# Performance work log

Measured on AMD Instinct MI355X. Metric: run time of the kernel, lower is better.

The kernel has to match this reference:

```python
import jax, jax.numpy as jnp
import numpy as np
import math

D = 128       # d_model (file-scope constant)
L_LEN = 128   # length; forced == d_model by the un-transposed attention call
NH = 4        # n_head
DK = D // NH
K = 7         # depthwise conv kernel size
LC = 4        # conv_num
EPS = 1e-5    # LayerNorm eps
NEG = -1e30


def _pos_encoding():
    i = np.arange(D).astype(np.float64)
    freqs = np.where(i % 2 == 0, 10000.0 ** (-i / D), -(10000.0 ** ((1 - i) / D)))
    phases = np.where(i % 2 == 0, 0.0, math.pi / 2)
    pos = np.arange(L_LEN).astype(np.float64)[None, :]          # (1, L)
    pe = np.sin(pos * freqs[:, None] + phases[:, None])          # (D, L)
    return jnp.asarray(pe, jnp.float32)

PE = _pos_encoding()


def layernorm2d(x, w, b):
    # LayerNorm over the trailing (D, L) dims jointly, elementwise affine (D, L)
    mu = x.mean(axis=(-2, -1), keepdims=True)
    var = x.var(axis=(-2, -1), keepdims=True)
    return (x - mu) * jax.lax.rsqrt(var + EPS) * w + b


def sep_conv(x, dw_w, dw_b, pw_w, pw_b):
    # depthwise conv1d (groups=C) then 1x1 pointwise conv. x: (B, C, L)
    h = jax.lax.conv_general_dilated(
        x, dw_w[:, None, :], window_strides=(1,), padding=[(K // 2, K // 2)],
        dimension_numbers=('NCH', 'OIH', 'NCH'), feature_group_count=D)
    h = h + dw_b[:, None]
    return jnp.einsum('bcl,oc->bol', h, pw_w) + pw_b[:, None]


def mha(x, mask_f, Wq, bq, Wk, bk, Wv, bv, Wo, bo):
    # x: (B, Lx, F) with Lx == F == D here (module feeds (B, d_model, length) untransposed)
    B, Lx, _ = x.shape
    q = (x @ Wq.T + bq).reshape(B, Lx, NH, DK)
    k = (x @ Wk.T + bk).reshape(B, Lx, NH, DK)
    v = (x @ Wv.T + bv).reshape(B, Lx, NH, DK)
    scores = jnp.einsum('bqhd,bkhd->bhqk', q, k) * (1.0 / math.sqrt(DK))
    m = mask_f[:, None, None, :]                         # (B,1,1,Lx)
    scores = scores * (1.0 - m) + m * NEG                # mask_logits
    attn = jax.nn.softmax(scores, axis=-1)
    out = jnp.einsum('bhqk,bkhd->bqhd', attn, v).reshape(B, Lx, D)
    return out @ Wo.T + bo


def setup_inputs() -> dict:
    key = jax.random.key(0)
    ks = jax.random.split(key, 16)
    B = 1024
    s = 0.02
    inp = {
        'x': jax.random.normal(ks[0], (B, D, L_LEN), jnp.float32),
        'mask': jax.random.randint(ks[1], (B, L_LEN), 0, 2, jnp.int32),
        'dw_w': jax.random.normal(ks[2], (LC, D, K), jnp.float32) * s,
        'dw_b': jnp.zeros((LC, D), jnp.float32),
        'pw_w': jax.random.normal(ks[3], (LC, D, D), jnp.float32) * s,
        'pw_b': jnp.zeros((LC, D), jnp.float32),
        'normb_w': jnp.ones((D, L_LEN), jnp.float32),
        'normb_b': jnp.zeros((D, L_LEN), jnp.float32),
        'norms_w': jnp.ones((LC, D, L_LEN), jnp.float32),
        'norms_b': jnp.zeros((LC, D, L_LEN), jnp.float32),
        'norme_w': jnp.ones((D, L_LEN), jnp.float32),
        'norme_b': jnp.zeros((D, L_LEN), jnp.float32),
        'Wq': jax.random.normal(ks[4], (D, D), jnp.float32) * s,
        'bq': jnp.zeros((D,), jnp.float32),
        'Wk': jax.random.normal(ks[5], (D, D), jnp.float32) * s,
        'bk': jnp.zeros((D,), jnp.float32),
        'Wv': jax.random.normal(ks[6], (D, D), jnp.float32) * s,
        'bv': jnp.zeros((D,), jnp.float32),
        'Wo': jax.random.normal(ks[7], (D, D), jnp.float32) * s,
        'bo': jnp.zeros((D,), jnp.float32),
        'fc_w': jax.random.normal(ks[8], (D, D), jnp.float32) * s,
        'fc_b': jnp.zeros((D,), jnp.float32),
    }
    return inp


def reference(x, mask, dw_w, dw_b, pw_w, pw_b, normb_w, normb_b, norms_w, norms_b,
              norme_w, norme_b, Wq, bq, Wk, bk, Wv, bv, Wo, bo, fc_w, fc_b):
    # Eval mode: all dropouts are identity.
    mask_f = mask.astype(x.dtype)
    out = x + PE                                  # PosEncoder
    res = out
    out = layernorm2d(out, normb_w, normb_b)      # normb
    for i in range(LC):                           # fixed small layer loop
        h = sep_conv(out, dw_w[i], dw_b[i], pw_w[i], pw_b[i])
        out = jax.nn.relu(h) + res
        res = out
        out = layernorm2d(out, norms_w[i], norms_b[i])
    att = mha(out, mask_f, Wq, bq, Wk, bk, Wv, bv, Wo, bo)
    out = att + res
    res = out
    out = layernorm2d(out, norme_w, norme_b)
    # fc applied over channel dim: (B,C,L)->(B,L,C) linear ->(B,C,L)
    h = jnp.einsum('bcl,oc->bol', out, fc_w) + fc_b[:, None]
    out = jax.nn.relu(h) + res
    return out
```

## Files before the change

### kernel.cpp

```cpp
#include <hip/hip_runtime.h>

#define NEGF -1e30f
#define EPSF 1e-5f

typedef __attribute__((ext_vector_type(8))) short bf16x8;
typedef __attribute__((ext_vector_type(4))) float f32x4;
typedef unsigned short u16;
typedef unsigned int u32;

#define WSU_PW 0
#define WSU_FC 65536
#define WSU_WO 81920
#define WSU_WQ 98304
#define WSU_WK 114688
#define WSU_WV 131072
#define WSU_END 147456

__device__ __forceinline__ u16 f2bf(float x) {
  u32 u = __float_as_uint(x);
  u += 0x7fffu + ((u >> 16) & 1u);
  return (u16)(u >> 16);
}
__device__ __forceinline__ float bf2f(u16 u) {
  return __uint_as_float(((u32)u) << 16);
}
__device__ __forceinline__ f32x4 mfma16(bf16x8 a, bf16x8 b, f32x4 c) {
  return __builtin_amdgcn_mfma_f32_16x16x32_bf16(a, b, c, 0, 0, 0);
}
__device__ __forceinline__ void mm_frags(const u16* base, bf16x8* f) {
  f[0] = *(const bf16x8*)(base);
  f[1] = *(const bf16x8*)(base + 32);
  f[2] = *(const bf16x8*)(base + 64);
  f[3] = *(const bf16x8*)(base + 96);
}

__global__ __launch_bounds__(128) void prep_kernel(
    const float* __restrict__ pw_w, const float* __restrict__ fc_w,
    const float* __restrict__ Wo, const float* __restrict__ Wq,
    const float* __restrict__ Wk, const float* __restrict__ Wv,
    u16* __restrict__ wsu) {
  int job = blockIdx.x, r = blockIdx.y, c = threadIdx.x;
  int idx = r * 128 + c;
  if (job < 4)       wsu[WSU_PW + job * 16384 + idx] = f2bf(pw_w[job * 16384 + idx]);
  else if (job == 4) wsu[WSU_FC + idx] = f2bf(fc_w[idx]);
  else if (job == 5) wsu[WSU_WO + idx] = f2bf(Wo[idx]);
  else if (job == 6) wsu[WSU_WQ + idx] = f2bf(Wq[idx]);
  else if (job == 7) wsu[WSU_WK + idx] = f2bf(Wk[idx]);
  else if (job == 8) wsu[WSU_WV + idx] = f2bf(Wv[idx]);
  else {
    float* pe = (float*)(wsu + WSU_END);
    int d = r, pos = c;
    double freq, phase;
    if ((d & 1) == 0) { freq = pow(10000.0, -(double)d / 128.0); phase = 0.0; }
    else { freq = -pow(10000.0, (1.0 - (double)d) / 128.0); phase = 1.5707963267948966; }
    pe[d * 128 + pos] = (float)sin((double)pos * freq + phase);
  }
}

__device__ __forceinline__ void ln_stats(const float* resv, float* red, int t,
                                         float& mu, float& inv) {
  float s = 0.f, s2 = 0.f;
#pragma unroll
  for (int i = 0; i < 16; i++) { float v = resv[i]; s += v; s2 += v * v; }
#pragma unroll
  for (int off = 32; off > 0; off >>= 1) {
    s += __shfl_down(s, off, 64);
    s2 += __shfl_down(s2, off, 64);
  }
  if ((t & 63) == 0) { red[(t >> 6) * 2] = s; red[(t >> 6) * 2 + 1] = s2; }
  __syncthreads();
  float S = 0.f, S2 = 0.f;
#pragma unroll
  for (int i = 0; i < 16; i++) { S += red[2 * i]; S2 += red[2 * i + 1]; }
  mu = S * (1.0f / 16384.0f);
  float var = S2 * (1.0f / 16384.0f) - mu * mu;
  inv = rsqrtf(var + EPSF);
}

__global__ __launch_bounds__(1024) void enc_kernel(
    const float* __restrict__ x, const int* __restrict__ mask,
    const float* __restrict__ dw_w, const float* __restrict__ dw_b,
    const float* __restrict__ pw_b,
    const float* __restrict__ normb_w, const float* __restrict__ normb_b,
    const float* __restrict__ norms_w, const float* __restrict__ norms_b,
    const float* __restrict__ norme_w, const float* __restrict__ norme_b,
    const float* __restrict__ bq, const float* __restrict__ bk,
    const float* __restrict__ bv, const float* __restrict__ bo,
    const float* __restrict__ fc_b, const u16* __restrict__ wsu,
    const float* __restrict__ pe, float* __restrict__ out) {
  __shared__ __align__(16) u16 A_raw[128 * 136 + 16];
  __shared__ __align__(16) u16 VTb[32 * 136];
  __shared__ float EX[512];
  __shared__ float mask_s[128];
  __shared__ float red[32];
  u16* A = A_raw + 8;
  u16* QH = A;
  u16* KH = A + 5120;
  u16* PN = A;

  const int t = threadIdx.x;
  const int b = blockIdx.x;
  const int lane = t & 63;
  const int r16 = lane & 15;
  const int quad = lane >> 4;
  const int wv = t >> 6;
  const int m0 = __builtin_amdgcn_readfirstlane((wv >> 1) << 4);
  const int nh = __builtin_amdgcn_readfirstlane(wv & 1);
  const int l = t & 127;
  const int og = __builtin_amdgcn_readfirstlane(t >> 7);
  const int obase = og << 4;
  const int dup = __builtin_amdgcn_readfirstlane(wv >> 3);
  const int mq0 = __builtin_amdgcn_readfirstlane((wv & 7) << 4);

  if (t < 128) mask_s[t] = (float)mask[b * 128 + t];

  float res[16];
  {
    const float* xb = x + (size_t)b * 16384;
#pragma unroll
    for (int i = 0; i < 16; i++) {
      int o = obase + i;
      res[i] = xb[o * 128 + l] + pe[o * 128 + l];
    }
  }
  {
    float mu, inv;
    ln_stats(res, red, t, mu, inv);
#pragma unroll
    for (int i = 0; i < 16; i++) {
      int o = obase + i;
      A[o * 136 + l] = f2bf((res[i] - mu) * inv * normb_w[o * 128 + l] + normb_b[o * 128 + l]);
    }
    __syncthreads();
  }

#pragma unroll 1
  for (int layer = 0; layer < 4; layer++) {
    {
      const float* dwp = dw_w + layer * 896 + l * 7;
      float wreg[7];
#pragma unroll
      for (int j = 0; j < 7; j++) wreg[j] = dwp[j];
      float bias = dw_b[layer * 128 + l];
      const u16* xrow = A + l * 136;
      const int lb = og << 4;
      bf16x8 vz = {0, 0, 0, 0, 0, 0, 0, 0};
      bf16x8 v0 = (lb == 0) ? vz : *(const bf16x8*)(xrow + lb - 8);
      bf16x8 v1 = *(const bf16x8*)(xrow + lb);
      bf16x8 v2 = *(const bf16x8*)(xrow + lb + 8);
      bf16x8 v3 = (lb == 112) ? vz : *(const bf16x8*)(xrow + lb + 16);
      __syncthreads();
#pragma unroll
      for (int k = 0; k < 2; k++) {
        bf16x8 vp = k ? v1 : v0;
        bf16x8 vc = k ? v2 : v1;
        bf16x8 vn = k ? v3 : v2;
        float w14[14];
        w14[0] = bf2f((u16)vp[5]); w14[1] = bf2f((u16)vp[6]); w14[2] = bf2f((u16)vp[7]);
#pragma unroll
        for (int j = 0; j < 8; j++) w14[3 + j] = bf2f((u16)vc[j]);
        w14[11] = bf2f((u16)vn[0]); w14[12] = bf2f((u16)vn[1]); w14[13] = bf2f((u16)vn[2]);
        const int lb2 = lb + 8 * k;
#pragma unroll
        for (int j = 0; j < 8; j++) {
          float a = bias;
#pragma unroll
          for (int tt = 0; tt < 7; tt++) a += w14[j + tt] * wreg[tt];
          A[(lb2 + j) * 136 + l] = f2bf(a);
        }
      }
    }
    __syncthreads();
    {
      const u16* pwp = wsu + WSU_PW + (layer << 14) + (m0 + r16) * 128 + quad * 8;
      bf16x8 a[4];
      mm_frags(pwp, a);
      f32x4 c4[4];
#pragma unroll
      for (int ni = 0; ni < 4; ni++) {
        int n = nh * 4 + ni;
        const u16* hb = A + (16 * n + r16) * 136 + quad * 8;
        f32x4 c = {0.f, 0.f, 0.f, 0.f};
        c = mfma16(a[0], *(const bf16x8*)(hb), c);
        c = mfma16(a[1], *(const bf16x8*)(hb + 32), c);
        c = mfma16(a[2], *(const bf16x8*)(hb + 64), c);
        c = mfma16(a[3], *(const bf16x8*)(hb + 96), c);
        c4[ni] = c;
      }
      __syncthreads();
#pragma unroll
      for (int ni = 0; ni < 4; ni++) {
        int n = nh * 4 + ni;
        u16* sp = A + (m0 + quad * 4) * 136 + 16 * n + r16;
        sp[0] = f2bf(c4[ni][0]); sp[136] = f2bf(c4[ni][1]);
        sp[272] = f2bf(c4[ni][2]); sp[408] = f2bf(c4[ni][3]);
      }
    }
    __syncthreads();
    {
#pragma unroll
      for (int i = 0; i < 16; i++)
        res[i] += fmaxf(bf2f(A[(obase + i) * 136 + l]) + pw_b[layer * 128 + obase + i], 0.f);
      float mu, inv;
      ln_stats(res, red, t, mu, inv);
      const float* wg = norms_w + layer * 16384;
      const float* bg = norms_b + layer * 16384;
#pragma unroll
      for (int i = 0; i < 16; i++) {
        int o = obase + i;
        A[o * 136 + l] = f2bf((res[i] - mu) * inv * wg[o * 128 + l] + bg[o * 128 + l]);
      }
      __syncthreads();
    }
  }

  bf16x8 xf[4];
  mm_frags(A + (m0 + r16) * 136 + quad * 8, xf);
  __syncthreads();

  u32 att32[8];
#pragma unroll 1
  for (int hd = 0; hd < 4; hd++) {
    {
      const int j2 = nh * 16 + r16;
      const int jrow = hd * 32 + j2;
      {
        bf16x8 w[4];
        mm_frags(wsu + WSU_WQ + jrow * 128 + quad * 8, w);
        f32x4 c = {0.f, 0.f, 0.f, 0.f};
        c = mfma16(xf[0], w[0], c); c = mfma16(xf[1], w[1], c);
        c = mfma16(xf[2], w[2], c); c = mfma16(xf[3], w[3], c);
        float bb = bq[jrow];
#pragma unroll
        for (int r = 0; r < 4; r++)
          QH[(m0 + quad * 4 + r) * 40 + j2] = f2bf((c[r] + bb) * 0.17677669529663687f);
      }
      {
        bf16x8 w[4];
        mm_frags(wsu + WSU_WK + jrow * 128 + quad * 8, w);
        f32x4 c = {0.f, 0.f, 0.f, 0.f};
        c = mfma16(xf[0], w[0], c); c = mfma16(xf[1], w[1], c);
        c = mfma16(xf[2], w[2], c); c = mfma16(xf[3], w[3], c);
        float bb = bk[jrow];
#pragma unroll
        for (int r = 0; r < 4; r++)
          KH[(m0 + quad * 4 + r) * 40 + j2] = f2bf(c[r] + bb);
      }
      {
        bf16x8 w[4];
        mm_frags(wsu + WSU_WV + jrow * 128 + quad * 8, w);
        f32x4 c = {0.f, 0.f, 0.f, 0.f};
        c = mfma16(xf[0], w[0], c); c = mfma16(xf[1], w[1], c);
        c = mfma16(xf[2], w[2], c); c = mfma16(xf[3], w[3], c);
        float bb = bv[jrow];
        u32 lo = (u32)f2bf(c[0] + bb) | ((u32)f2bf(c[1] + bb) << 16);
        u32 hi = (u32)f2bf(c[2] + bb) | ((u32)f2bf(c[3] + bb) << 16);
        u16* vp = VTb + j2 * 136 + m0 + quad * 4;
        *(u32*)(vp) = lo;
        *(u32*)(vp + 2) = hi;
      }
    }
    __syncthreads();
    f32x4 sc[4];
    {
      bf16x8 aq = *(const bf16x8*)(QH + (mq0 + r16) * 40 + quad * 8);
#pragma unroll
      for (int ni = 0; ni < 4; ni++) {
        f32x4 z = {0.f, 0.f, 0.f, 0.f};
        sc[ni] = mfma16(aq, *(const bf16x8*)(KH + ((dup * 4 + ni) * 16 + r16) * 40 + quad * 8), z);
      }
#pragma unroll
      for (int ni = 0; ni < 4; ni++) {
        float mv = mask_s[(dup * 4 + ni) * 16 + r16];
        if (mv > 0.5f) { sc[ni][0] = NEGF; sc[ni][1] = NEGF; sc[ni][2] = NEGF; sc[ni][3] = NEGF; }
      }
    }
    float mxr[4];
#pragma unroll
    for (int r = 0; r < 4; r++) {
      float mx = fmaxf(fmaxf(sc[0][r], sc[1][r]), fmaxf(sc[2][r], sc[3][r]));
      mx = fmaxf(mx, __shfl_xor(mx, 1, 64));
      mx = fmaxf(mx, __shfl_xor(mx, 2, 64));
      mx = fmaxf(mx, __shfl_xor(mx, 4, 64));
      mx = fmaxf(mx, __shfl_xor(mx, 8, 64));
      if (r16 == 0) EX[dup * 128 + mq0 + quad * 4 + r] = mx;
      mxr[r] = mx;
    }
    __syncthreads();
    float ps[4];
#pragma unroll
    for (int r = 0; r < 4; r++) {
      const int row = mq0 + quad * 4 + r;
      float fm = fmaxf(mxr[r], EX[(dup ^ 1) * 128 + row]);
      float s = 0.f;
      u16* pp2 = PN + row * 136 + r16;
#pragma unroll
      for (int ni = 0; ni < 4; ni++) {
        float p = __expf(sc[ni][r] - fm);
        pp2[(dup * 4 + ni) * 16] = f2bf(p);
        s += p;
      }
      s += __shfl_xor(s, 1, 64);
      s += __shfl_xor(s, 2, 64);
      s += __shfl_xor(s, 4, 64);
      s += __shfl_xor(s, 8, 64);
      if (r16 == 0) EX[256 + dup * 128 + row] = s;
      ps[r] = s;
    }
    __syncthreads();
    {
      const u16* pq = PN + (mq0 + r16) * 136 + quad * 8;
      const u16* vb = VTb + (dup * 16 + r16) * 136 + quad * 8;
      f32x4 c = {0.f, 0.f, 0.f, 0.f};
      c = mfma16(*(const bf16x8*)(pq), *(const bf16x8*)(vb), c);
      c = mfma16(*(const bf16x8*)(pq + 32), *(const bf16x8*)(vb + 32), c);
      c = mfma16(*(const bf16x8*)(pq + 64), *(const bf16x8*)(vb + 64), c);
      c = mfma16(*(const bf16x8*)(pq + 96), *(const bf16x8*)(vb + 96), c);
      float v0 = c[0] / (ps[0] + EX[256 + (dup ^ 1) * 128 + mq0 + quad * 4 + 0]);
      float v1 = c[1] / (ps[1] + EX[256 + (dup ^ 1) * 128 + mq0 + quad * 4 + 1]);
      float v2 = c[2] / (ps[2] + EX[256 + (dup ^ 1) * 128 + mq0 + quad * 4 + 2]);
      float v3 = c[3] / (ps[3] + EX[256 + (dup ^ 1) * 128 + mq0 + quad * 4 + 3]);
      att32[hd * 2 + 0] = (u32)f2bf(v0) | ((u32)f2bf(v1) << 16);
      att32[hd * 2 + 1] = (u32)f2bf(v2) | ((u32)f2bf(v3) << 16);
    }
    __syncthreads();
  }

#pragma unroll
  for (int hd = 0; hd < 4; hd++)
#pragma unroll
    for (int i = 0; i < 2; i++)
#pragma unroll
      for (int h = 0; h < 2; h++)
        A[(mq0 + quad * 4 + 2 * i + h) * 136 + hd * 32 + dup * 16 + r16] =
            (u16)(att32[hd * 2 + i] >> (16 * h));
  __syncthreads();
  {
    const u16* ap = A + (m0 + r16) * 136 + quad * 8;
    bf16x8 a4[4];
    mm_frags(ap, a4);
    f32x4 c4[4];
#pragma unroll
    for (int ni = 0; ni < 4; ni++) {
      int n = nh * 4 + ni;
      bf16x8 w[4];
      mm_frags(wsu + WSU_WO + (16 * n + r16) * 128 + quad * 8, w);
      f32x4 c = {0.f, 0.f, 0.f, 0.f};
      c = mfma16(a4[0], w[0], c); c = mfma16(a4[1], w[1], c);
      c = mfma16(a4[2], w[2], c); c = mfma16(a4[3], w[3], c);
      c4[ni] = c;
    }
    __syncthreads();
#pragma unroll
    for (int ni = 0; ni < 4; ni++) {
      int n = nh * 4 + ni;
      u16* sp = A + (m0 + quad * 4) * 136 + 16 * n + r16;
      sp[0] = f2bf(c4[ni][0]); sp[136] = f2bf(c4[ni][1]);
      sp[272] = f2bf(c4[ni][2]); sp[408] = f2bf(c4[ni][3]);
    }
  }
  __syncthreads();
  {
    float bol = bo[l];
#pragma unroll
    for (int i = 0; i < 16; i++) res[i] += bf2f(A[(obase + i) * 136 + l]) + bol;
    float mu, inv;
    ln_stats(res, red, t, mu, inv);
#pragma unroll
    for (int i = 0; i < 16; i += 2) {
      int o = obase + i;
      float v0 = (res[i] - mu) * inv * norme_w[o * 128 + l] + norme_b[o * 128 + l];
      float v1 = (res[i + 1] - mu) * inv * norme_w[(o + 1) * 128 + l] + norme_b[(o + 1) * 128 + l];
      *(u32*)(A + l * 136 + o) = (u32)f2bf(v0) | ((u32)f2bf(v1) << 16);
    }
    __syncthreads();
  }
  {
    const u16* fp = wsu + WSU_FC + (m0 + r16) * 128 + quad * 8;
    bf16x8 a4[4];
    mm_frags(fp, a4);
    f32x4 c4[4];
#pragma unroll
    for (int ni = 0; ni < 4; ni++) {
      int n = nh * 4 + ni;
      const u16* hb = A + (16 * n + r16) * 136 + quad * 8;
      f32x4 c = {0.f, 0.f, 0.f, 0.f};
      c = mfma16(a4[0], *(const bf16x8*)(hb), c);
      c = mfma16(a4[1], *(const bf16x8*)(hb + 32), c);
      c = mfma16(a4[2], *(const bf16x8*)(hb + 64), c);
      c = mfma16(a4[3], *(const bf16x8*)(hb + 96), c);
      c4[ni] = c;
    }
    __syncthreads();
#pragma unroll
    for (int ni = 0; ni < 4; ni++) {
      int n = nh * 4 + ni;
      u16* sp = A + (m0 + quad * 4) * 136 + 16 * n + r16;
      sp[0] = f2bf(c4[ni][0]); sp[136] = f2bf(c4[ni][1]);
      sp[272] = f2bf(c4[ni][2]); sp[408] = f2bf(c4[ni][3]);
    }
  }
  __syncthreads();
  {
    float* outb = out + (size_t)b * 16384;
#pragma unroll
    for (int i = 0; i < 16; i++) {
      float hv = bf2f(A[(obase + i) * 136 + l]) + fc_b[obase + i];
      outb[(obase + i) * 128 + l] = fmaxf(hv, 0.f) + res[i];
    }
  }
}

extern "C" void kernel_launch(void* const* d_in, const int* in_sizes, int n_in,
                              void* d_out, int out_size, void* d_ws, size_t ws_size,
                              hipStream_t stream) {
  const float* x       = (const float*)d_in[0];
  const int*   mask    = (const int*)d_in[1];
  const float* dw_w    = (const float*)d_in[2];
  const float* dw_b    = (const float*)d_in[3];
  const float* pw_w    = (const float*)d_in[4];
  const float* pw_b    = (const float*)d_in[5];
  const float* normb_w = (const float*)d_in[6];
  const float* normb_b = (const float*)d_in[7];
  const float* norms_w = (const float*)d_in[8];
  const float* norms_b = (const float*)d_in[9];
  const float* norme_w = (const float*)d_in[10];
  const float* norme_b = (const float*)d_in[11];
  const float* Wq      = (const float*)d_in[12];
  const float* bq      = (const float*)d_in[13];
  const float* Wk      = (const float*)d_in[14];
  const float* bk      = (const float*)d_in[15];
  const float* Wv      = (const float*)d_in[16];
  const float* bv      = (const float*)d_in[17];
  const float* Wo      = (const float*)d_in[18];
  const float* bo      = (const float*)d_in[19];
  const float* fc_w    = (const float*)d_in[20];
  const float* fc_b    = (const float*)d_in[21];
  float* out = (float*)d_out;
  u16* wsu = (u16*)d_ws;
  const float* pe = (const float*)(wsu + WSU_END);
  int B = in_sizes[0] / 16384;

  prep_kernel<<<dim3(10, 128), dim3(128), 0, stream>>>(pw_w, fc_w, Wo, Wq, Wk, Wv, wsu);
  enc_kernel<<<dim3(B), dim3(1024), 0, stream>>>(
      x, mask, dw_w, dw_b, pw_b, normb_w, normb_b, norms_w, norms_b,
      norme_w, norme_b, bq, bk, bv, bo, fc_b, wsu, pe, out);
}
```

Measured before the change: 644.4 us.

## Process two batch elements per block to amortize barriers and weight fragments

Each 1024-thread block now handles two batch samples at once, with duplicated LDS buffers (activations, conv scratch, V^T, softmax stats, masks). Every stage is interleaved across both samples: LayerNorm reductions share one barrier, the depthwise conv writes to separate scratch buffers so a barrier is dropped, and GEMM weight fragments (pointwise, QKV, Wo, fc) are loaded once and reused for both samples. The aim is to halve barrier and weight-load overhead per sample and give each wave more independent MFMA work. In exchange LDS use roughly doubles and register pressure rises, which may reduce occupancy or cause spills, and the grid is halved to 512 blocks.

```diff
diff --git a/kernel.cpp b/kernel.cpp
--- a/kernel.cpp
+++ b/kernel.cpp
@@ -57,24 +57,248 @@
   }
 }
 
-__device__ __forceinline__ void ln_stats(const float* resv, float* red, int t,
-                                         float& mu, float& inv) {
-  float s = 0.f, s2 = 0.f;
-#pragma unroll
-  for (int i = 0; i < 16; i++) { float v = resv[i]; s += v; s2 += v * v; }
+__device__ __forceinline__ void ln_stats2(const float* r0, const float* r1,
+                                          float* red0, float* red1, int t,
+                                          float& mu0, float& inv0,
+                                          float& mu1, float& inv1) {
+  float s0 = 0.f, q0 = 0.f, s1 = 0.f, q1 = 0.f;
+#pragma unroll
+  for (int i = 0; i < 16; i++) {
+    float a = r0[i], b = r1[i];
+    s0 += a; q0 += a * a; s1 += b; q1 += b * b;
+  }
 #pragma unroll
   for (int off = 32; off > 0; off >>= 1) {
-    s += __shfl_down(s, off, 64);
-    s2 += __shfl_down(s2, off, 64);
-  }
-  if ((t & 63) == 0) { red[(t >> 6) * 2] = s; red[(t >> 6) * 2 + 1] = s2; }
+    s0 += __shfl_down(s0, off, 64); q0 += __shfl_down(q0, off, 64);
+    s1 += __shfl_down(s1, off, 64); q1 += __shfl_down(q1, off, 64);
+  }
+  if ((t & 63) == 0) {
+    int w = t >> 6;
+    red0[w * 2] = s0; red0[w * 2 + 1] = q0;
+    red1[w * 2] = s1; red1[w * 2 + 1] = q1;
+  }
   __syncthreads();
-  float S = 0.f, S2 = 0.f;
-#pragma unroll
-  for (int i = 0; i < 16; i++) { S += red[2 * i]; S2 += red[2 * i + 1]; }
-  mu = S * (1.0f / 16384.0f);
-  float var = S2 * (1.0f / 16384.0f) - mu * mu;
-  inv = rsqrtf(var + EPSF);
+  float S0 = 0.f, Q0 = 0.f, S1 = 0.f, Q1 = 0.f;
+#pragma unroll
+  for (int i = 0; i < 16; i++) {
+    S0 += red0[2 * i]; Q0 += red0[2 * i + 1];
+    S1 += red1[2 * i]; Q1 += red1[2 * i + 1];
+  }
+  mu0 = S0 * (1.0f / 16384.0f);
+  float v0 = Q0 * (1.0f / 16384.0f) - mu0 * mu0; inv0 = rsqrtf(v0 + EPSF);
+  mu1 = S1 * (1.0f / 16384.0f);
+  float v1 = Q1 * (1.0f / 16384.0f) - mu1 * mu1; inv1 = rsqrtf(v1 + EPSF);
+}
+
+__device__ __forceinline__ void dw_conv(const u16* A, u16* XS, const float* wreg,
+                                        float bias, int og, int l) {
+  const u16* xrow = A + l * 136;
+  const int lb = og << 4;
+  bf16x8 vz = {0, 0, 0, 0, 0, 0, 0, 0};
+  bf16x8 v0 = (lb == 0) ? vz : *(const bf16x8*)(xrow + lb - 8);
+  bf16x8 v1 = *(const bf16x8*)(xrow + lb);
+  bf16x8 v2 = *(const bf16x8*)(xrow + lb + 8);
+  bf16x8 v3 = (lb == 112) ? vz : *(const bf16x8*)(xrow + lb + 16);
+#pragma unroll
+  for (int k = 0; k < 2; k++) {
+    bf16x8 vp = k ? v1 : v0;
+    bf16x8 vc = k ? v2 : v1;
+    bf16x8 vn = k ? v3 : v2;
+    float w14[14];
+    w14[0] = bf2f((u16)vp[5]); w14[1] = bf2f((u16)vp[6]); w14[2] = bf2f((u16)vp[7]);
+#pragma unroll
+    for (int j = 0; j < 8; j++) w14[3 + j] = bf2f((u16)vc[j]);
+    w14[11] = bf2f((u16)vn[0]); w14[12] = bf2f((u16)vn[1]); w14[13] = bf2f((u16)vn[2]);
+    const int lb2 = lb + 8 * k;
+#pragma unroll
+    for (int j = 0; j < 8; j++) {
+      float a = bias;
+#pragma unroll
+      for (int tt = 0; tt < 7; tt++) a += w14[j + tt] * wreg[tt];
+      XS[(lb2 + j) * 136 + l] = f2bf(a);
+    }
+  }
+}
+
+__device__ __forceinline__ void gemm_stage2(const u16* aB, int aS,
+                                            const u16* b0B, const u16* b1B, int bS,
+                                            u16* d0, u16* d1,
+                                            int m0, int nh, int r16, int quad) {
+  bf16x8 a[4];
+  mm_frags(aB + (m0 + r16) * aS + quad * 8, a);
+#pragma unroll
+  for (int ni = 0; ni < 4; ni++) {
+    int n = nh * 4 + ni;
+    {
+      bf16x8 w[4];
+      mm_frags(b0B + (16 * n + r16) * bS + quad * 8, w);
+      f32x4 c = {0.f, 0.f, 0.f, 0.f};
+      c = mfma16(a[0], w[0], c); c = mfma16(a[1], w[1], c);
+      c = mfma16(a[2], w[2], c); c = mfma16(a[3], w[3], c);
+      u16* sp = d0 + (m0 + quad * 4) * 136 + 16 * n + r16;
+      sp[0] = f2bf(c[0]); sp[136] = f2bf(c[1]); sp[272] = f2bf(c[2]); sp[408] = f2bf(c[3]);
+    }
+    {
+      bf16x8 w[4];
+      mm_frags(b1B + (16 * n + r16) * bS + quad * 8, w);
+      f32x4 c = {0.f, 0.f, 0.f, 0.f};
+      c = mfma16(a[0], w[0], c); c = mfma16(a[1], w[1], c);
+      c = mfma16(a[2], w[2], c); c = mfma16(a[3], w[3], c);
+      u16* sp = d1 + (m0 + quad * 4) * 136 + 16 * n + r16;
+      sp[0] = f2bf(c[0]); sp[136] = f2bf(c[1]); sp[272] = f2bf(c[2]); sp[408] = f2bf(c[3]);
+    }
+  }
+}
+
+__device__ __forceinline__ void gemm_stage2b(const u16* a0B, const u16* a1B, int aS,
+                                             const u16* bB, int bS,
+                                             u16* d0, u16* d1,
+                                             int m0, int nh, int r16, int quad) {
+  bf16x8 a0[4], a1[4];
+  mm_frags(a0B + (m0 + r16) * aS + quad * 8, a0);
+  mm_frags(a1B + (m0 + r16) * aS + quad * 8, a1);
+#pragma unroll
+  for (int ni = 0; ni < 4; ni++) {
+    int n = nh * 4 + ni;
+    bf16x8 w[4];
+    mm_frags(bB + (16 * n + r16) * bS + quad * 8, w);
+    {
+      f32x4 c = {0.f, 0.f, 0.f, 0.f};
+      c = mfma16(a0[0], w[0], c); c = mfma16(a0[1], w[1], c);
+      c = mfma16(a0[2], w[2], c); c = mfma16(a0[3], w[3], c);
+      u16* sp = d0 + (m0 + quad * 4) * 136 + 16 * n + r16;
+      sp[0] = f2bf(c[0]); sp[136] = f2bf(c[1]); sp[272] = f2bf(c[2]); sp[408] = f2bf(c[3]);
+    }
+    {
+      f32x4 c = {0.f, 0.f, 0.f, 0.f};
+      c = mfma16(a1[0], w[0], c); c = mfma16(a1[1], w[1], c);
+      c = mfma16(a1[2], w[2], c); c = mfma16(a1[3], w[3], c);
+      u16* sp = d1 + (m0 + quad * 4) * 136 + 16 * n + r16;
+      sp[0] = f2bf(c[0]); sp[136] = f2bf(c[1]); sp[272] = f2bf(c[2]); sp[408] = f2bf(c[3]);
+    }
+  }
+}
+
+__device__ __forceinline__ void qkv2(const u16* XS0, const u16* XS1,
+                                     u16* QH0, u16* QH1, u16* KH0, u16* KH1,
+                                     u16* VT0, u16* VT1,
+                                     const u16* wsu, int jrow,
+                                     float bqv, float bkv, float bvv,
+                                     int m0, int j2, int r16, int quad) {
+  bf16x8 x0[4], x1[4];
+  mm_frags(XS0 + (m0 + r16) * 136 + quad * 8, x0);
+  mm_frags(XS1 + (m0 + r16) * 136 + quad * 8, x1);
+  {
+    bf16x8 w[4];
+    mm_frags(wsu + WSU_WQ + jrow * 128 + quad * 8, w);
+    f32x4 c0 = {0.f, 0.f, 0.f, 0.f}, c1 = {0.f, 0.f, 0.f, 0.f};
+    c0 = mfma16(x0[0], w[0], c0); c0 = mfma16(x0[1], w[1], c0);
+    c0 = mfma16(x0[2], w[2], c0); c0 = mfma16(x0[3], w[3], c0);
+    c1 = mfma16(x1[0], w[0], c1); c1 = mfma16(x1[1], w[1], c1);
+    c1 = mfma16(x1[2], w[2], c1); c1 = mfma16(x1[3], w[3], c1);
+#pragma unroll
+    for (int r = 0; r < 4; r++) {
+      QH0[(m0 + quad * 4 + r) * 40 + j2] = f2bf((c0[r] + bqv) * 0.17677669529663687f);
+      QH1[(m0 + quad * 4 + r) * 40 + j2] = f2bf((c1[r] + bqv) * 0.17677669529663687f);
+    }
+  }
+  {
+    bf16x8 w[4];
+    mm_frags(wsu + WSU_WK + jrow * 128 + quad * 8, w);
+    f32x4 c0 = {0.f, 0.f, 0.f, 0.f}, c1 = {0.f, 0.f, 0.f, 0.f};
+    c0 = mfma16(x0[0], w[0], c0); c0 = mfma16(x0[1], w[1], c0);
+    c0 = mfma16(x0[2], w[2], c0); c0 = mfma16(x0[3], w[3], c0);
+    c1 = mfma16(x1[0], w[0], c1); c1 = mfma16(x1[1], w[1], c1);
+    c1 = mfma16(x1[2], w[2], c1); c1 = mfma16(x1[3], w[3], c1);
+#pragma unroll
+    for (int r = 0; r < 4; r++) {
+      KH0[(m0 + quad * 4 + r) * 40 + j2] = f2bf(c0[r] + bkv);
+      KH1[(m0 + quad * 4 + r) * 40 + j2] = f2bf(c1[r] + bkv);
+    }
+  }
+  {
+    bf16x8 w[4];
+    mm_frags(wsu + WSU_WV + jrow * 128 + quad * 8, w);
+    f32x4 c0 = {0.f, 0.f, 0.f, 0.f}, c1 = {0.f, 0.f, 0.f, 0.f};
+    c0 = mfma16(x0[0], w[0], c0); c0 = mfma16(x0[1], w[1], c0);
+    c0 = mfma16(x0[2], w[2], c0); c0 = mfma16(x0[3], w[3], c0);
+    c1 = mfma16(x1[0], w[0], c1); c1 = mfma16(x1[1], w[1], c1);
+    c1 = mfma16(x1[2], w[2], c1); c1 = mfma16(x1[3], w[3], c1);
+    u16* vp0 = VT0 + j2 * 136 + m0 + quad * 4;
+    u16* vp1 = VT1 + j2 * 136 + m0 + quad * 4;
+    *(u32*)(vp0) = (u32)f2bf(c0[0] + bvv) | ((u32)f2bf(c0[1] + bvv) << 16);
+    *(u32*)(vp0 + 2) = (u32)f2bf(c0[2] + bvv) | ((u32)f2bf(c0[3] + bvv) << 16);
+    *(u32*)(vp1) = (u32)f2bf(c1[0] + bvv) | ((u32)f2bf(c1[1] + bvv) << 16);
+    *(u32*)(vp1 + 2) = (u32)f2bf(c1[2] + bvv) | ((u32)f2bf(c1[3] + bvv) << 16);
+  }
+}
+
+__device__ __forceinline__ void mha_scores(const u16* QH, const u16* KH, const float* msk,
+                                           float* EX, int dup, int mq0, int r16, int quad,
+                                           f32x4 (&sc)[4], float (&mxr)[4]) {
+  bf16x8 aq = *(const bf16x8*)(QH + (mq0 + r16) * 40 + quad * 8);
+#pragma unroll
+  for (int ni = 0; ni < 4; ni++) {
+    f32x4 z = {0.f, 0.f, 0.f, 0.f};
+    sc[ni] = mfma16(aq, *(const bf16x8*)(KH + ((dup * 4 + ni) * 16 + r16) * 40 + quad * 8), z);
+  }
+#pragma unroll
+  for (int ni = 0; ni < 4; ni++) {
+    float mv = msk[(dup * 4 + ni) * 16 + r16];
+    if (mv > 0.5f) { sc[ni][0] = NEGF; sc[ni][1] = NEGF; sc[ni][2] = NEGF; sc[ni][3] = NEGF; }
+  }
+#pragma unroll
+  for (int r = 0; r < 4; r++) {
+    float mx = fmaxf(fmaxf(sc[0][r], sc[1][r]), fmaxf(sc[2][r], sc[3][r]));
+    mx = fmaxf(mx, __shfl_xor(mx, 1, 64));
+    mx = fmaxf(mx, __shfl_xor(mx, 2, 64));
+    mx = fmaxf(mx, __shfl_xor(mx, 4, 64));
+    mx = fmaxf(mx, __shfl_xor(mx, 8, 64));
+    if (r16 == 0) EX[dup * 128 + mq0 + quad * 4 + r] = mx;
+    mxr[r] = mx;
+  }
+}
+
+__device__ __forceinline__ void mha_exp(u16* PN, float* EX, const f32x4 (&sc)[4],
+                                        const float (&mxr)[4], int dup, int mq0,
+                                        int r16, int quad, float (&ps)[4]) {
+#pragma unroll
+  for (int r = 0; r < 4; r++) {
+    const int row = mq0 + quad * 4 + r;
+    float fm = fmaxf(mxr[r], EX[(dup ^ 1) * 128 + row]);
+    float s = 0.f;
+    u16* pp = PN + row * 136 + r16;
+#pragma unroll
+    for (int ni = 0; ni < 4; ni++) {
+      float p = __expf(sc[ni][r] - fm);
+      pp[(dup * 4 + ni) * 16] = f2bf(p);
+      s += p;
+    }
+    s += __shfl_xor(s, 1, 64);
+    s += __shfl_xor(s, 2, 64);
+    s += __shfl_xor(s, 4, 64);
+    s += __shfl_xor(s, 8, 64);
+    if (r16 == 0) EX[256 + dup * 128 + row] = s;
+    ps[r] = s;
+  }
+}
+
+__device__ __forceinline__ void mha_pv(const u16* PN, const u16* VT, const float* EX,
+                                       const float (&ps)[4], int dup, int mq0,
+                                       int r16, int quad, u32& alo, u32& ahi) {
+  const u16* pq = PN + (mq0 + r16) * 136 + quad * 8;
+  const u16* vb = VT + (dup * 16 + r16) * 136 + quad * 8;
+  f32x4 c = {0.f, 0.f, 0.f, 0.f};
+  c = mfma16(*(const bf16x8*)(pq), *(const bf16x8*)(vb), c);
+  c = mfma16(*(const bf16x8*)(pq + 32), *(const bf16x8*)(vb + 32), c);
+  c = mfma16(*(const bf16x8*)(pq + 64), *(const bf16x8*)(vb + 64), c);
+  c = mfma16(*(const bf16x8*)(pq + 96), *(const bf16x8*)(vb + 96), c);
+  float v0 = c[0] / (ps[0] + EX[256 + (dup ^ 1) * 128 + mq0 + quad * 4 + 0]);
+  float v1 = c[1] / (ps[1] + EX[256 + (dup ^ 1) * 128 + mq0 + quad * 4 + 1]);
+  float v2 = c[2] / (ps[2] + EX[256 + (dup ^ 1) * 128 + mq0 + quad * 4 + 2]);
+  float v3 = c[3] / (ps[3] + EX[256 + (dup ^ 1) * 128 + mq0 + quad * 4 + 3]);
+  alo = (u32)f2bf(v0) | ((u32)f2bf(v1) << 16);
+  ahi = (u32)f2bf(v2) | ((u32)f2bf(v3) << 16);
 }
 
 __global__ __launch_bounds__(1024) void enc_kernel(
@@ -87,19 +311,25 @@
     const float* __restrict__ bq, const float* __restrict__ bk,
     const float* __restrict__ bv, const float* __restrict__ bo,
     const float* __restrict__ fc_b, const u16* __restrict__ wsu,
-    const float* __restrict__ pe, float* __restrict__ out) {
-  __shared__ __align__(16) u16 A_raw[128 * 136 + 16];
-  __shared__ __align__(16) u16 VTb[32 * 136];
-  __shared__ float EX[512];
-  __shared__ float mask_s[128];
-  __shared__ float red[32];
-  u16* A = A_raw + 8;
-  u16* QH = A;
-  u16* KH = A + 5120;
-  u16* PN = A;
+    const float* __restrict__ pe, float* __restrict__ out, int B) {
+  __shared__ __align__(16) u16 A0_raw[128 * 136 + 16];
+  __shared__ __align__(16) u16 A1_raw[128 * 136 + 16];
+  __shared__ __align__(16) u16 XS0[128 * 136];
+  __shared__ __align__(16) u16 XS1[128 * 136];
+  __shared__ __align__(16) u16 VT0[32 * 136];
+  __shared__ __align__(16) u16 VT1[32 * 136];
+  __shared__ float EX0[512], EX1[512];
+  __shared__ float msk0[128], msk1[128];
+  __shared__ float red0[32], red1[32];
+  u16* A0 = A0_raw + 8;
+  u16* A1 = A1_raw + 8;
+  u16* QH0 = A0; u16* KH0 = A0 + 5120; u16* PN0 = A0;
+  u16* QH1 = A1; u16* KH1 = A1 + 5120; u16* PN1 = A1;
 
   const int t = threadIdx.x;
-  const int b = blockIdx.x;
+  const int b0 = 2 * blockIdx.x;
+  const int b1 = b0 + 1;
+  const bool has1 = (b1 < B);
   const int lane = t & 63;
   const int r16 = lane & 15;
   const int quad = lane >> 4;
@@ -112,24 +342,32 @@
   const int dup = __builtin_amdgcn_readfirstlane(wv >> 3);
   const int mq0 = __builtin_amdgcn_readfirstlane((wv & 7) << 4);
 
-  if (t < 128) mask_s[t] = (float)mask[b * 128 + t];
-
-  float res[16];
-  {
-    const float* xb = x + (size_t)b * 16384;
+  if (t < 128) {
+    msk0[t] = (float)mask[b0 * 128 + t];
+    msk1[t] = has1 ? (float)mask[b1 * 128 + t] : 0.f;
+  }
+
+  float res0[16], res1[16];
+  {
+    const float* xb0 = x + (size_t)b0 * 16384;
+    const float* xb1 = x + (size_t)b1 * 16384;
 #pragma unroll
     for (int i = 0; i < 16; i++) {
       int o = obase + i;
-      res[i] = xb[o * 128 + l] + pe[o * 128 + l];
-    }
-  }
-  {
-    float mu, inv;
-    ln_stats(res, red, t, mu, inv);
+      float p = pe[o * 128 + l];
+      res0[i] = xb0[o * 128 + l] + p;
+      res1[i] = has1 ? (xb1[o * 128 + l] + p) : 0.f;
+    }
+  }
+  {
+    float mu0, inv0, mu1, inv1;
+    ln_stats2(res0, res1, red0, red1, t, mu0, inv0, mu1, inv1);
 #pragma unroll
     for (int i = 0; i < 16; i++) {
       int o = obase + i;
-      A[o * 136 + l] = f2bf((res[i] - mu) * inv * normb_w[o * 128 + l] + normb_b[o * 128 + l]);
+      float w_ = normb_w[o * 128 + l], bb = normb_b[o * 128 + l];
+      A0[o * 136 + l] = f2bf((res0[i] - mu0) * inv0 * w_ + bb);
+      A1[o * 136 + l] = f2bf((res1[i] - mu1) * inv1 * w_ + bb);
     }
     __syncthreads();
   }
@@ -142,271 +380,114 @@
 #pragma unroll
       for (int j = 0; j < 7; j++) wreg[j] = dwp[j];
       float bias = dw_b[layer * 128 + l];
-      const u16* xrow = A + l * 136;
-      const int lb = og << 4;
-      bf16x8 vz = {0, 0, 0, 0, 0, 0, 0, 0};
-      bf16x8 v0 = (lb == 0) ? vz : *(const bf16x8*)(xrow + lb - 8);
-      bf16x8 v1 = *(const bf16x8*)(xrow + lb);
-      bf16x8 v2 = *(const bf16x8*)(xrow + lb + 8);
-      bf16x8 v3 = (lb == 112) ? vz : *(const bf16x8*)(xrow + lb + 16);
-      __syncthreads();
-#pragma unroll
-      for (int k = 0; k < 2; k++) {
-        bf16x8 vp = k ? v1 : v0;
-        bf16x8 vc = k ? v2 : v1;
-        bf16x8 vn = k ? v3 : v2;
-        float w14[14];
-        w14[0] = bf2f((u16)vp[5]); w14[1] = bf2f((u16)vp[6]); w14[2] = bf2f((u16)vp[7]);
-#pragma unroll
-        for (int j = 0; j < 8; j++) w14[3 + j] = bf2f((u16)vc[j]);
-        w14[11] = bf2f((u16)vn[0]); w14[12] = bf2f((u16)vn[1]); w14[13] = bf2f((u16)vn[2]);
-        const int lb2 = lb + 8 * k;
-#pragma unroll
-        for (int j = 0; j < 8; j++) {
-          float a = bias;
-#pragma unroll
-          for (int tt = 0; tt < 7; tt++) a += w14[j + tt] * wreg[tt];
-          A[(lb2 + j) * 136 + l] = f2bf(a);
-        }
+      dw_conv(A0, XS0, wreg, bias, og, l);
+      dw_conv(A1, XS1, wreg, bias, og, l);
+    }
+    __syncthreads();
+    gemm_stage2(wsu + WSU_PW + (layer << 14), 128, XS0, XS1, 136, A0, A1,
+                m0, nh, r16, quad);
+    __syncthreads();
+    {
+      u16* t0 = (layer == 3) ? XS0 : A0;
+      u16* t1 = (layer == 3) ? XS1 : A1;
+#pragma unroll
+      for (int i = 0; i < 16; i++) {
+        float pb = pw_b[layer * 128 + obase + i];
+        res0[i] += fmaxf(bf2f(A0[(obase + i) * 136 + l]) + pb, 0.f);
+        res1[i] += fmaxf(bf2f(A1[(obase + i) * 136 + l]) + pb, 0.f);
       }
-    }
-    __syncthreads();
-    {
-      const u16* pwp = wsu + WSU_PW + (layer << 14) + (m0 + r16) * 128 + quad * 8;
-      bf16x8 a[4];
-      mm_frags(pwp, a);
-      f32x4 c4[4];
-#pragma unroll
-      for (int ni = 0; ni < 4; ni++) {
-        int n = nh * 4 + ni;
-        const u16* hb = A + (16 * n + r16) * 136 + quad * 8;
-        f32x4 c = {0.f, 0.f, 0.f, 0.f};
-        c = mfma16(a[0], *(const bf16x8*)(hb), c);
-        c = mfma16(a[1], *(const bf16x8*)(hb + 32), c);
-        c = mfma16(a[2], *(const bf16x8*)(hb + 64), c);
-        c = mfma16(a[3], *(const bf16x8*)(hb + 96), c);
-        c4[ni] = c;
+      float mu0, inv0, mu1, inv1;
+      ln_stats2(res0, res1, red0, red1, t, mu0, inv0, mu1, inv1);
+      const float* wg = norms_w + layer * 16384;
+      const float* bg = norms_b + layer * 16384;
+#pragma unroll
+      for (int i = 0; i < 16; i++) {
+        int o = obase + i;
+        float w_ = wg[o * 128 + l], bb = bg[o * 128 + l];
+        t0[o * 136 + l] = f2bf((res0[i] - mu0) * inv0 * w_ + bb);
+        t1[o * 136 + l] = f2bf((res1[i] - mu1) * inv1 * w_ + bb);
       }
       __syncthreads();
-#pragma unroll
-      for (int ni = 0; ni < 4; ni++) {
-        int n = nh * 4 + ni;
-        u16* sp = A + (m0 + quad * 4) * 136 + 16 * n + r16;
-        sp[0] = f2bf(c4[ni][0]); sp[136] = f2bf(c4[ni][1]);
-        sp[272] = f2bf(c4[ni][2]); sp[408] = f2bf(c4[ni][3]);
-      }
-    }
-    __syncthreads();
-    {
-#pragma unroll
-      for (int i = 0; i < 16; i++)
-        res[i] += fmaxf(bf2f(A[(obase + i) * 136 + l]) + pw_b[layer * 128 + obase + i], 0.f);
-      float mu, inv;
-      ln_stats(res, red, t, mu, inv);
-      const float* wg = norms_w + layer * 16384;
-      const float* bg = norms_b + layer * 16384;
-#pragma unroll
-      for (int i = 0; i < 16; i++) {
-        int o = obase + i;
-        A[o * 136 + l] = f2bf((res[i] - mu) * inv * wg[o * 128 + l] + bg[o * 128 + l]);
-      }
-      __syncthreads();
-    }
-  }
-
-  bf16x8 xf[4];
-  mm_frags(A + (m0 + r16) * 136 + quad * 8, xf);
-  __syncthreads();
-
-  u32 att32[8];
-#pragma unroll 1
+    }
+  }
+
+  u32 at0lo[4], at0hi[4], at1lo[4], at1hi[4];
+#pragma unroll
   for (int hd = 0; hd < 4; hd++) {
     {
       const int j2 = nh * 16 + r16;
       const int jrow = hd * 32 + j2;
-      {
-        bf16x8 w[4];
-        mm_frags(wsu + WSU_WQ + jrow * 128 + quad * 8, w);
-        f32x4 c = {0.f, 0.f, 0.f, 0.f};
-        c = mfma16(xf[0], w[0], c); c = mfma16(xf[1], w[1], c);
-        c = mfma16(xf[2], w[2], c); c = mfma16(xf[3], w[3], c);
-        float bb = bq[jrow];
-#pragma unroll
-        for (int r = 0; r < 4; r++)
-          QH[(m0 + quad * 4 + r) * 40 + j2] = f2bf((c[r] + bb) * 0.17677669529663687f);
-      }
-      {
-        bf16x8 w[4];
-        mm_frags(wsu + WSU_WK + jrow * 128 + quad * 8, w);
-        f32x4 c = {0.f, 0.f, 0.f, 0.f};
-        c = mfma16(xf[0], w[0], c); c = mfma16(xf[1], w[1], c);
-        c = mfma16(xf[2], w[2], c); c = mfma16(xf[3], w[3], c);
-        float bb = bk[jrow];
-#pragma unroll
-        for (int r = 0; r < 4; r++)
-          KH[(m0 + quad * 4 + r) * 40 + j2] = f2bf(c[r] + bb);
-      }
-      {
-        bf16x8 w[4];
-        mm_frags(wsu + WSU_WV + jrow * 128 + quad * 8, w);
-        f32x4 c = {0.f, 0.f, 0.f, 0.f};
-        c = mfma16(xf[0], w[0], c); c = mfma16(xf[1], w[1], c);
-        c = mfma16(xf[2], w[2], c); c = mfma16(xf[3], w[3], c);
-        float bb = bv[jrow];
-        u32 lo = (u32)f2bf(c[0] + bb) | ((u32)f2bf(c[1] + bb) << 16);
-        u32 hi = (u32)f2bf(c[2] + bb) | ((u32)f2bf(c[3] + bb) << 16);
-        u16* vp = VTb + j2 * 136 + m0 + quad * 4;
-        *(u32*)(vp) = lo;
-        *(u32*)(vp + 2) = hi;
-      }
-    }
-    __syncthreads();
-    f32x4 sc[4];
-    {
-      bf16x8 aq = *(const bf16x8*)(QH + (mq0 + r16) * 40 + quad * 8);
-#pragma unroll
-      for (int ni = 0; ni < 4; ni++) {
-        f32x4 z = {0.f, 0.f, 0.f, 0.f};
-        sc[ni] = mfma16(aq, *(const bf16x8*)(KH + ((dup * 4 + ni) * 16 + r16) * 40 + quad * 8), z);
-      }
-#pragma unroll
-      for (int ni = 0; ni < 4; ni++) {
-        float mv = mask_s[(dup * 4 + ni) * 16 + r16];
-        if (mv > 0.5f) { sc[ni][0] = NEGF; sc[ni][1] = NEGF; sc[ni][2] = NEGF; sc[ni][3] = NEGF; }
-      }
-    }
-    float mxr[4];
-#pragma unroll
-    for (int r = 0; r < 4; r++) {
-      float mx = fmaxf(fmaxf(sc[0][r], sc[1][r]), fmaxf(sc[2][r], sc[3][r]));
-      mx = fmaxf(mx, __shfl_xor(mx, 1, 64));
-      mx = fmaxf(mx, __shfl_xor(mx, 2, 64));
-      mx = fmaxf(mx, __shfl_xor(mx, 4, 64));
-      mx = fmaxf(mx, __shfl_xor(mx, 8, 64));
-      if (r16 == 0) EX[dup * 128 + mq0 + quad * 4 + r] = mx;
-      mxr[r] = mx;
-    }
-    __syncthreads();
-    float ps[4];
-#pragma unroll
-    for (int r = 0; r < 4; r++) {
-      const int row = mq0 + quad * 4 + r;
-      float fm = fmaxf(mxr[r], EX[(dup ^ 1) * 128 + row]);
-      float s = 0.f;
-      u16* pp2 = PN + row * 136 + r16;
-#pragma unroll
-      for (int ni = 0; ni < 4; ni++) {
-        float p = __expf(sc[ni][r] - fm);
-        pp2[(dup * 4 + ni) * 16] = f2bf(p);
-        s += p;
-      }
-      s += __shfl_xor(s, 1, 64);
-      s += __shfl_xor(s, 2, 64);
-      s += __shfl_xor(s, 4, 64);
-      s += __shfl_xor(s, 8, 64);
-      if (r16 == 0) EX[256 + dup * 128 + row] = s;
-      ps[r] = s;
-    }
-    __syncthreads();
-    {
-      const u16* pq = PN + (mq0 + r16) * 136 + quad * 8;
-      const u16* vb = VTb + (dup * 16 + r16) * 136 + quad * 8;
-      f32x4 c = {0.f, 0.f, 0.f, 0.f};
-      c = mfma16(*(const bf16x8*)(pq), *(const bf16x8*)(vb), c);
-      c = mfma16(*(const bf16x8*)(pq + 32), *(const bf16x8*)(vb + 32), c);
-      c = mfma16(*(const bf16x8*)(pq + 64), *(const bf16x8*)(vb + 64), c);
-      c = mfma16(*(const bf16x8*)(pq + 96), *(const bf16x8*)(vb + 96), c);
-      float v0 = c[0] / (ps[0] + EX[256 + (dup ^ 1) * 128 + mq0 + quad * 4 + 0]);
-      float v1 = c[1] / (ps[1] + EX[256 + (dup ^ 1) * 128 + mq0 + quad * 4 + 1]);
-      float v2 = c[2] / (ps[2] + EX[256 + (dup ^ 1) * 128 + mq0 + quad * 4 + 2]);
-      float v3 = c[3] / (ps[3] + EX[256 + (dup ^ 1) * 128 + mq0 + quad * 4 + 3]);
-      att32[hd * 2 + 0] = (u32)f2bf(v0) | ((u32)f2bf(v1) << 16);
-      att32[hd * 2 + 1] = (u32)f2bf(v2) | ((u32)f2bf(v3) << 16);
-    }
-    __syncthreads();
-  }
-
-#pragma unroll
-  for (int hd = 0; hd < 4; hd++)
-#pragma unroll
-    for (int i = 0; i < 2; i++)
-#pragma unroll
-      for (int h = 0; h < 2; h++)
-        A[(mq0 + quad * 4 + 2 * i + h) * 136 + hd * 32 + dup * 16 + r16] =
-            (u16)(att32[hd * 2 + i] >> (16 * h));
+      qkv2(XS0, XS1, QH0, QH1, KH0, KH1, VT0, VT1, wsu, jrow,
+           bq[jrow], bk[jrow], bv[jrow], m0, j2, r16, quad);
+    }
+    __syncthreads();
+    f32x4 sc0[4], sc1[4];
+    float mx0[4], mx1[4];
+    mha_scores(QH0, KH0, msk0, EX0, dup, mq0, r16, quad, sc0, mx0);
+    mha_scores(QH1, KH1, msk1, EX1, dup, mq0, r16, quad, sc1, mx1);
+    __syncthreads();
+    float ps0[4], ps1[4];
+    mha_exp(PN0, EX0, sc0, mx0, dup, mq0, r16, quad, ps0);
+    mha_exp(PN1, EX1, sc1, mx1, dup, mq0, r16, quad, ps1);
+    __syncthreads();
+    mha_pv(PN0, VT0, EX0, ps0, dup, mq0, r16, quad, at0lo[hd], at0hi[hd]);
+    mha_pv(PN1, VT1, EX1, ps1, dup, mq0, r16, quad, at1lo[hd], at1hi[hd]);
+    __syncthreads();
+  }
+
+#pragma unroll
+  for (int hd = 0; hd < 4; hd++) {
+    int col = hd * 32 + dup * 16 + r16;
+    A0[(mq0 + quad * 4 + 0) * 136 + col] = (u16)(at0lo[hd]);
+    A0[(mq0 + quad * 4 + 1) * 136 + col] = (u16)(at0lo[hd] >> 16);
+    A0[(mq0 + quad * 4 + 2) * 136 + col] = (u16)(at0hi[hd]);
+    A0[(mq0 + quad * 4 + 3) * 136 + col] = (u16)(at0hi[hd] >> 16);
+    A1[(mq0 + quad * 4 + 0) * 136 + col] = (u16)(at1lo[hd]);
+    A1[(mq0 + quad * 4 + 1) * 136 + col] = (u16)(at1lo[hd] >> 16);
+    A1[(mq0 + quad * 4 + 2) * 136 + col] = (u16)(at1hi[hd]);
+    A1[(mq0 + quad * 4 + 3) * 136 + col] = (u16)(at1hi[hd] >> 16);
+  }
   __syncthreads();
-  {
-    const u16* ap = A + (m0 + r16) * 136 + quad * 8;
-    bf16x8 a4[4];
-    mm_frags(ap, a4);
-    f32x4 c4[4];
-#pragma unroll
-    for (int ni = 0; ni < 4; ni++) {
-      int n = nh * 4 + ni;
-      bf16x8 w[4];
-      mm_frags(wsu + WSU_WO + (16 * n + r16) * 128 + quad * 8, w);
-      f32x4 c = {0.f, 0.f, 0.f, 0.f};
-      c = mfma16(a4[0], w[0], c); c = mfma16(a4[1], w[1], c);
-      c = mfma16(a4[2], w[2], c); c = mfma16(a4[3], w[3], c);
-      c4[ni] = c;
-    }
-    __syncthreads();
-#pragma unroll
-    for (int ni = 0; ni < 4; ni++) {
-      int n = nh * 4 + ni;
-      u16* sp = A + (m0 + quad * 4) * 136 + 16 * n + r16;
-      sp[0] = f2bf(c4[ni][0]); sp[136] = f2bf(c4[ni][1]);
-      sp[272] = f2bf(c4[ni][2]); sp[408] = f2bf(c4[ni][3]);
-    }
-  }
+  gemm_stage2b(A0, A1, 136, wsu + WSU_WO, 128, XS0, XS1, m0, nh, r16, quad);
   __syncthreads();
   {
     float bol = bo[l];
 #pragma unroll
-    for (int i = 0; i < 16; i++) res[i] += bf2f(A[(obase + i) * 136 + l]) + bol;
-    float mu, inv;
-    ln_stats(res, red, t, mu, inv);
+    for (int i = 0; i < 16; i++) {
+      res0[i] += bf2f(XS0[(obase + i) * 136 + l]) + bol;
+      res1[i] += bf2f(XS1[(obase + i) * 136 + l]) + bol;
+    }
+    float mu0, inv0, mu1, inv1;
+    ln_stats2(res0, res1, red0, red1, t, mu0, inv0, mu1, inv1);
 #pragma unroll
     for (int i = 0; i < 16; i += 2) {
       int o = obase + i;
-      float v0 = (res[i] - mu) * inv * norme_w[o * 128 + l] + norme_b[o * 128 + l];
-      float v1 = (res[i + 1] - mu) * inv * norme_w[(o + 1) * 128 + l] + norme_b[(o + 1) * 128 + l];
-      *(u32*)(A + l * 136 + o) = (u32)f2bf(v0) | ((u32)f2bf(v1) << 16);
-    }
-    __syncthreads();
-  }
-  {
-    const u16* fp = wsu + WSU_FC + (m0 + r16) * 128 + quad * 8;
-    bf16x8 a4[4];
-    mm_frags(fp, a4);
-    f32x4 c4[4];
-#pragma unroll
-    for (int ni = 0; ni < 4; ni++) {
-      int n = nh * 4 + ni;
-      const u16* hb = A + (16 * n + r16) * 136 + quad * 8;
-      f32x4 c = {0.f, 0.f, 0.f, 0.f};
-      c = mfma16(a4[0], *(const bf16x8*)(hb), c);
-      c = mfma16(a4[1], *(const bf16x8*)(hb + 32), c);
-      c = mfma16(a4[2], *(const bf16x8*)(hb + 64), c);
-      c = mfma16(a4[3], *(const bf16x8*)(hb + 96), c);
-      c4[ni] = c;
-    }
-    __syncthreads();
-#pragma unroll
-    for (int ni = 0; ni < 4; ni++) {
-      int n = nh * 4 + ni;
-      u16* sp = A + (m0 + quad * 4) * 136 + 16 * n + r16;
-      sp[0] = f2bf(c4[ni][0]); sp[136] = f2bf(c4[ni][1]);
-      sp[272] = f2bf(c4[ni][2]); sp[408] = f2bf(c4[ni][3]);
-    }
-  }
+      float wa = norme_w[o * 128 + l], ba = norme_b[o * 128 + l];
+      float wb = norme_w[(o + 1) * 128 + l], bb = norme_b[(o + 1) * 128 + l];
+      float u0 = (res0[i] - mu0) * inv0 * wa + ba;
+      float u1 = (res0[i + 1] - mu0) * inv0 * wb + bb;
+      *(u32*)(A0 + l * 136 + o) = (u32)f2bf(u0) | ((u32)f2bf(u1) << 16);
+      float v0 = (res1[i] - mu1) * inv1 * wa + ba;
+      float v1 = (res1[i + 1] - mu1) * inv1 * wb + bb;
+      *(u32*)(A1 + l * 136 + o) = (u32)f2bf(v0) | ((u32)f2bf(v1) << 16);
+    }
+    __syncthreads();
+  }
+  gemm_stage2(wsu + WSU_FC, 128, A0, A1, 136, XS0, XS1, m0, nh, r16, quad);
   __syncthreads();
   {
-    float* outb = out + (size_t)b * 16384;
+    float* ob0 = out + (size_t)b0 * 16384;
+    float* ob1 = out + (size_t)b1 * 16384;
 #pragma unroll
     for (int i = 0; i < 16; i++) {
-      float hv = bf2f(A[(obase + i) * 136 + l]) + fc_b[obase + i];
-      outb[(obase + i) * 128 + l] = fmaxf(hv, 0.f) + res[i];
+      int o = obase + i;
+      float fb = fc_b[o];
+      float h0 = bf2f(XS0[o * 136 + l]) + fb;
+      ob0[o * 128 + l] = fmaxf(h0, 0.f) + res0[i];
+      if (has1) {
+        float h1 = bf2f(XS1[o * 136 + l]) + fb;
+        ob1[o * 128 + l] = fmaxf(h1, 0.f) + res1[i];
+      }
     }
   }
 }
@@ -442,7 +523,7 @@
   int B = in_sizes[0] / 16384;
 
   prep_kernel<<<dim3(10, 128), dim3(128), 0, stream>>>(pw_w, fc_w, Wo, Wq, Wk, Wv, wsu);
-  enc_kernel<<<dim3(B), dim3(1024), 0, stream>>>(
+  enc_kernel<<<dim3((B + 1) / 2), dim3(1024), 0, stream>>>(
       x, mask, dw_w, dw_b, pw_b, normb_w, normb_b, norms_w, norms_b,
-      norme_w, norme_b, bq, bk, bv, bo, fc_b, wsu, pe, out);
-}
+      norme_w, norme_b, bq, bk, bv, bo, fc_b, wsu, pe, out, B);
+}
```

After: 602.3 us. -6.5%, faster.
